# Optimization experiments

Measured on AMD Instinct MI355X. Metric: run time of the kernel, lower is better.

Reference implementation:

```python
import jax, jax.numpy as jnp
import numpy as np

B = 4096


def setup_inputs() -> dict:
    key = jax.random.key(0)
    u = jax.random.uniform(key, (B, 5), dtype=jnp.float32)
    centers = u[:, :2] * 64.0          # box centers in [0, 64)
    wh = u[:, 2:4] * 8.0 + 1.0         # widths/heights in [1, 9)
    ang = u[:, 4:5] * 3.14159265       # rotation angle in [0, pi)
    boxes = jnp.concatenate([centers, wh, ang], axis=-1)  # (B,5)
    return {"boxes": boxes}


def _rect_to_corners(boxes):
    # boxes: (B,5) = (x, y, w, h, theta) -> corners (B,4,2)
    unit = jnp.array([[-1.0, -1.0], [1.0, -1.0], [1.0, 1.0], [-1.0, 1.0]],
                     dtype=boxes.dtype)
    ctr, wh, ang = boxes[:, :2], boxes[:, 2:4], boxes[:, 4]
    base = unit[None, :, :] * (wh * 0.5)[:, None, :]        # (B,4,2)
    c, s = jnp.cos(ang), jnp.sin(ang)
    rot = jnp.stack([jnp.stack([c, -s], -1),
                     jnp.stack([s, c], -1)], axis=1)         # (B,2,2)
    return jnp.einsum('bkd,bde->bke', base, rot) + ctr[:, None, :]


def _giou1d(min1, max1, min2, max2):
    # exact (non-fast) 1-D GIoU per axis
    inter = jnp.clip(jnp.minimum(max1, max2) - jnp.maximum(min1, min2), 0.0)
    union = (max1 - min1) + (max2 - min2) - inter
    hull = jnp.maximum(max1, max2) - jnp.minimum(min1, min2)
    return inter / union - (hull - union) / hull


def reference(boxes):
    corners = _rect_to_corners(boxes)                        # (B,4,2)
    nb = corners.shape[0]
    # two edge axes per box: c1-c0 and c3-c0
    axes = jnp.stack([corners[:, 1] - corners[:, 0],
                      corners[:, 3] - corners[:, 0]], axis=1)  # (B,2,2)
    # self projections: box b's corners onto its own axes
    sp = jnp.einsum('bkd,bad->bak', corners, axes)           # (B,2,4)
    smin, smax = sp.min(-1), sp.max(-1)                      # (B,2)
    # cross projections: corners of box i onto axes of box j
    cp = jnp.einsum('ikd,jad->ijak', corners, axes)          # (B,B,2,4)
    cmin, cmax = cp.min(-1), cp.max(-1)                      # (B,B,2)
    # projections of box j's corners onto box i's axes = transpose of cross
    cminT, cmaxT = jnp.swapaxes(cmin, 0, 1), jnp.swapaxes(cmax, 0, 1)
    # axes of box i: (box i self) vs (box j projected on i's axes)
    gA = _giou1d(smin[:, None, :], smax[:, None, :], cminT, cmaxT)  # (B,B,2)
    # axes of box j: (box i projected on j's axes) vs (box j self)
    gB = _giou1d(cmin, cmax, smin[None, :, :], smax[None, :, :])    # (B,B,2)
    g = jnp.concatenate([gA, gB], axis=-1).min(-1)           # min over 4 axes
    pairwise = jnp.clip(g, 0.0)
    idx = jnp.arange(nb)
    pairwise = pairwise.at[idx, idx].set(0.0)                # zero diagonal
    return pairwise  # reduction='none' -> (B,B)
```

## Files before the change

kernel.cpp:

```cpp
#include <hip/hip_runtime.h>
#include <math.h>

#define NBOX 4096
#define TILE 32
#define NT (NBOX / TILE)
#define NBLK (NT * (NT + 1) / 2)
#define SS 12
#define JB 400

typedef float v2f __attribute__((ext_vector_type(2)));
typedef float vf4 __attribute__((ext_vector_type(4)));


struct Box {
    v2f A0, A1, SC, LL;
    float cx, cy;
};

__device__ __forceinline__ float rcp_fast(float x) { return __builtin_amdgcn_rcpf(x); }
__device__ __forceinline__ v2f splat(float s) { return (v2f){s, s}; }
__device__ __forceinline__ v2f fma2(v2f a, v2f b, v2f c) { return __builtin_elementwise_fma(a, b, c); }
__device__ __forceinline__ v2f abs2(v2f a) { return __builtin_elementwise_abs(a); }

__device__ __forceinline__ float mgiou_pair(const Box& I, const Box& J) {
    v2f dA = fma2(I.A0, splat(J.A0.x), I.A1 * J.A1.x);
    v2f dB = fma2(I.A0, splat(J.A0.y), I.A1 * J.A1.y);
    v2f DI = fma2(I.A0, splat(J.cx), fma2(I.A1, splat(J.cy), -I.SC));
    v2f DJ = fma2(J.A0, splat(I.cx), fma2(J.A1, splat(I.cy), -J.SC));
    v2f aA = abs2(dA), aB = abs2(dB);
    v2f HI = aA + aB;
    float HJ0 = aA.x + aA.y;
    float HJ1 = aB.x + aB.y;
    v2f SI = I.LL + HI;
    float SJ0 = J.LL.x + HJ0, SJ1 = J.LL.y + HJ1;
    v2f uI = fma2(splat(0.5f), SI, -abs2(DI));
    float uJ0 = fmaf(0.5f, SJ0, -fabsf(DJ.x));
    float uJ1 = fmaf(0.5f, SJ1, -fabsf(DJ.y));
    float r0 = fminf(fminf(I.LL.x, HI.x), uI.x);
    float r1 = fminf(fminf(I.LL.y, HI.y), uI.y);
    float r2 = fminf(fminf(J.LL.x, HJ0), uJ0);
    float r3 = fminf(fminf(J.LL.y, HJ1), uJ1);
    float g0 = r0 * rcp_fast(SI.x - r0);
    float g1 = r1 * rcp_fast(SI.y - r1);
    float g2 = r2 * rcp_fast(SJ0 - r2);
    float g3 = r3 * rcp_fast(SJ1 - r3);
    float g = fminf(fminf(g0, g1), fminf(g2, g3));
    return fmaxf(g, 0.0f);
}

__device__ __forceinline__ int sw_offset(int i) { return i * SS + (i >> 3) * 4; }

__device__ __forceinline__ Box load_box(const float* p) {
    Box b;
    float4 x = *(const float4*)(p);
    float4 y = *(const float4*)(p + 4);
    float2 z = *(const float2*)(p + 8);
    b.A0 = (v2f){x.x, x.y}; b.A1 = (v2f){x.z, x.w};
    b.SC = (v2f){y.x, y.y}; b.LL = (v2f){y.z, y.w};
    b.cx = z.x; b.cy = z.y;
    return b;
}

__global__ __launch_bounds__(64)
void pairwise_kernel(const float* __restrict__ boxes, float* __restrict__ out) {
    int k = blockIdx.x;
    int bi = (int)((float)(2 * NT + 1 - sqrtf((float)((2 * NT + 1) * (2 * NT + 1) - 8 * k))) * 0.5f);
    if (bi > 0 && k < bi * NT - bi * (bi - 1) / 2) bi--;
    if (k >= (bi + 1) * NT - (bi + 1) * bi / 2) bi++;
    int bj = bi + (k - (bi * NT - bi * (bi - 1) / 2));

    __shared__ float sm[JB + 400];

    int tid = threadIdx.x;
    {
        int loc = tid & (TILE - 1);
        int box = ((tid < TILE) ? bi : bj) * TILE + loc;
        float cx = boxes[box * 5 + 0];
        float cy = boxes[box * 5 + 1];
        float w  = boxes[box * 5 + 2];
        float h  = boxes[box * 5 + 3];
        float ang = boxes[box * 5 + 4];
        float s, c;
        __sincosf(ang, &s, &c);
        float a0x = w * c, a0y = -w * s;
        float a1x = h * s, a1y =  h * c;
        float sc0 = fmaf(a0x, cx, a0y * cy);
        float sc1 = fmaf(a1x, cx, a1y * cy);
        float* d = &sm[((tid < TILE) ? 0 : JB) + sw_offset(loc)];
        ((float4*)d)[0] = make_float4(a0x, a1x, a0y, a1y);
        ((float4*)d)[1] = make_float4(sc0, sc1, w * w, h * h);
        ((float2*)d)[4] = make_float2(cx, cy);
    }
    __syncthreads();

    int tx = tid & 7;
    int ty = tid >> 3;
    Box J[4];
    const float* jp = &sm[JB + sw_offset(4 * tx)];
    #pragma unroll
    for (int m = 0; m < 4; ++m) J[m] = load_box(jp + m * SS);

    int ibase = bi * TILE, jbase = bj * TILE;
    bool offdiag = (bi != bj);
    const float* ip = &sm[sw_offset(4 * ty)];
    float vT[4][4];

    #pragma unroll
    for (int kk = 0; kk < 4; ++kk) {
        Box I = load_box(ip + kk * SS);
        int ig = ibase + 4 * ty + kk;
        float v[4];
        #pragma unroll
        for (int m = 0; m < 4; ++m) {
            int jg = jbase + 4 * tx + m;
            v[m] = (ig == jg) ? 0.0f : mgiou_pair(I, J[m]);
            vT[m][kk] = v[m];
        }
        vf4 o = {v[0], v[1], v[2], v[3]};
        *(vf4*)&out[(size_t)ig * NBOX + jbase + 4 * tx] = o;
    }

    if (offdiag) {
        #pragma unroll
        for (int m = 0; m < 4; ++m) {
            int jg = jbase + 4 * tx + m;
            vf4 o = {vT[m][0], vT[m][1], vT[m][2], vT[m][3]};
            *(vf4*)&out[(size_t)jg * NBOX + ibase + 4 * ty] = o;
        }
    }
}

extern "C" void kernel_launch(void* const* d_in, const int* in_sizes, int n_in,
                              void* d_out, int out_size, void* d_ws, size_t ws_size,
                              hipStream_t stream) {
    const float* boxes = (const float*)d_in[0];
    float* out = (float*)d_out;
    pairwise_kernel<<<dim3(NBLK), dim3(64), 0, stream>>>(boxes, out);
}
```

Before: 80.98 us.

## Enlarge tiles to 128 and transpose mirrored block through shared memory

Raises the tile to 128 boxes with 1024-thread blocks and writes the mirrored (transposed) half through an XOR-swizzled shared-memory staging buffer. Each row store then becomes a contiguous row segment instead of short 16-byte strided pieces. The aim is better-coalesced global writes for the 64 MB output and less per-block setup. In exchange it needs a second barrier, about 76 KB of shared memory per block, and leaves far fewer blocks (528), which may underfill the GPU's compute units.

```diff
diff --git a/kernel.cpp b/kernel.cpp
--- a/kernel.cpp
+++ b/kernel.cpp
@@ -2,11 +2,13 @@
 #include <math.h>
 
 #define NBOX 4096
-#define TILE 32
+#define TILE 128
 #define NT (NBOX / TILE)
 #define NBLK (NT * (NT + 1) / 2)
 #define SS 12
-#define JB 400
+#define BOXREG 1600
+#define JB BOXREG
+#define TB (2 * BOXREG)
 
 typedef float v2f __attribute__((ext_vector_type(2)));
 typedef float vf4 __attribute__((ext_vector_type(4)));
@@ -61,7 +63,9 @@
     return b;
 }
 
-__global__ __launch_bounds__(64)
+__device__ __forceinline__ int tidx(int r, int c) { return TB + r * TILE + (c ^ (r & 28)); }
+
+__global__ __launch_bounds__(1024)
 void pairwise_kernel(const float* __restrict__ boxes, float* __restrict__ out) {
     int k = blockIdx.x;
     int bi = (int)((float)(2 * NT + 1 - sqrtf((float)((2 * NT + 1) * (2 * NT + 1) - 8 * k))) * 0.5f);
@@ -69,10 +73,10 @@
     if (k >= (bi + 1) * NT - (bi + 1) * bi / 2) bi++;
     int bj = bi + (k - (bi * NT - bi * (bi - 1) / 2));
 
-    __shared__ float sm[JB + 400];
+    __shared__ float sm[TB + TILE * TILE];
 
     int tid = threadIdx.x;
-    {
+    if (tid < 2 * TILE) {
         int loc = tid & (TILE - 1);
         int box = ((tid < TILE) ? bi : bj) * TILE + loc;
         float cx = boxes[box * 5 + 0];
@@ -93,39 +97,47 @@
     }
     __syncthreads();
 
-    int tx = tid & 7;
-    int ty = tid >> 3;
+    int wave = tid >> 6;
+    int lane = tid & 63;
+    int jq = lane & 31;
+    int iset = lane >> 5;
+    int rloc = 8 * wave + 4 * iset;
+
     Box J[4];
-    const float* jp = &sm[JB + sw_offset(4 * tx)];
+    const float* jp = &sm[JB + sw_offset(4 * jq)];
     #pragma unroll
     for (int m = 0; m < 4; ++m) J[m] = load_box(jp + m * SS);
 
     int ibase = bi * TILE, jbase = bj * TILE;
-    bool offdiag = (bi != bj);
-    const float* ip = &sm[sw_offset(4 * ty)];
+    const float* ip = &sm[sw_offset(rloc)];
     float vT[4][4];
 
     #pragma unroll
     for (int kk = 0; kk < 4; ++kk) {
         Box I = load_box(ip + kk * SS);
-        int ig = ibase + 4 * ty + kk;
-        float v[4];
+        int ig = ibase + rloc + kk;
         #pragma unroll
         for (int m = 0; m < 4; ++m) {
-            int jg = jbase + 4 * tx + m;
-            v[m] = (ig == jg) ? 0.0f : mgiou_pair(I, J[m]);
-            vT[m][kk] = v[m];
+            int jg = jbase + 4 * jq + m;
+            vT[m][kk] = (ig == jg) ? 0.0f : mgiou_pair(I, J[m]);
         }
-        vf4 o = {v[0], v[1], v[2], v[3]};
-        *(vf4*)&out[(size_t)ig * NBOX + jbase + 4 * tx] = o;
+        vf4 o = {vT[0][kk], vT[1][kk], vT[2][kk], vT[3][kk]};
+        *(vf4*)&out[(size_t)ig * NBOX + jbase + 4 * jq] = o;
     }
 
-    if (offdiag) {
+    if (bi != bj) {
         #pragma unroll
         for (int m = 0; m < 4; ++m) {
-            int jg = jbase + 4 * tx + m;
-            vf4 o = {vT[m][0], vT[m][1], vT[m][2], vT[m][3]};
-            *(vf4*)&out[(size_t)jg * NBOX + ibase + 4 * ty] = o;
+            int r = 4 * jq + m;
+            *(vf4*)&sm[tidx(r, rloc)] = (vf4){vT[m][0], vT[m][1], vT[m][2], vT[m][3]};
+        }
+        __syncthreads();
+        int cq = 4 * jq;
+        #pragma unroll
+        for (int q = 0; q < 4; ++q) {
+            int r2 = 8 * wave + 4 * iset + q;
+            vf4 o = *(const vf4*)&sm[tidx(r2, cq)];
+            *(vf4*)&out[(size_t)(jbase + r2) * NBOX + ibase + cq] = o;
         }
     }
 }
@@ -135,5 +147,5 @@
                               hipStream_t stream) {
     const float* boxes = (const float*)d_in[0];
     float* out = (float*)d_out;
-    pairwise_kernel<<<dim3(NBLK), dim3(64), 0, stream>>>(boxes, out);
+    pairwise_kernel<<<dim3(NBLK), dim3(1024), 0, stream>>>(boxes, out);
 }
```

Result: slower. 91.80 us (+13.4%).

## Pack J-box pairs for packed-FP32 math and replace four reciprocals with one

Applied to the files above, without the earlier changes.

Stores J boxes in shared memory as interleaved pairs so each thread evaluates two pairs at once with v2f packed FMA/min/max across the J dimension. The four per-axis ratio computations r/(S-r) are replaced by cross-multiplying onto a common denominator, so only one reciprocal per pair is needed. The diagonal check moves under a block-level diag flag. The common-denominator products can lose precision or overflow for extreme sizes, and they add extra multiplies.

```diff
diff --git a/kernel.cpp b/kernel.cpp
--- a/kernel.cpp
+++ b/kernel.cpp
@@ -7,58 +7,82 @@
 #define NBLK (NT * (NT + 1) / 2)
 #define SS 12
 #define JB 400
+#define JPS 20
 
 typedef float v2f __attribute__((ext_vector_type(2)));
 typedef float vf4 __attribute__((ext_vector_type(4)));
-
-
-struct Box {
-    v2f A0, A1, SC, LL;
-    float cx, cy;
-};
 
 __device__ __forceinline__ float rcp_fast(float x) { return __builtin_amdgcn_rcpf(x); }
 __device__ __forceinline__ v2f splat(float s) { return (v2f){s, s}; }
 __device__ __forceinline__ v2f fma2(v2f a, v2f b, v2f c) { return __builtin_elementwise_fma(a, b, c); }
 __device__ __forceinline__ v2f abs2(v2f a) { return __builtin_elementwise_abs(a); }
+__device__ __forceinline__ v2f min2(v2f a, v2f b) { return __builtin_elementwise_min(a, b); }
+__device__ __forceinline__ v2f max2(v2f a, v2f b) { return __builtin_elementwise_max(a, b); }
 
-__device__ __forceinline__ float mgiou_pair(const Box& I, const Box& J) {
-    v2f dA = fma2(I.A0, splat(J.A0.x), I.A1 * J.A1.x);
-    v2f dB = fma2(I.A0, splat(J.A0.y), I.A1 * J.A1.y);
-    v2f DI = fma2(I.A0, splat(J.cx), fma2(I.A1, splat(J.cy), -I.SC));
-    v2f DJ = fma2(J.A0, splat(I.cx), fma2(J.A1, splat(I.cy), -J.SC));
-    v2f aA = abs2(dA), aB = abs2(dB);
-    v2f HI = aA + aB;
-    float HJ0 = aA.x + aA.y;
-    float HJ1 = aB.x + aB.y;
-    v2f SI = I.LL + HI;
-    float SJ0 = J.LL.x + HJ0, SJ1 = J.LL.y + HJ1;
-    v2f uI = fma2(splat(0.5f), SI, -abs2(DI));
-    float uJ0 = fmaf(0.5f, SJ0, -fabsf(DJ.x));
-    float uJ1 = fmaf(0.5f, SJ1, -fabsf(DJ.y));
-    float r0 = fminf(fminf(I.LL.x, HI.x), uI.x);
-    float r1 = fminf(fminf(I.LL.y, HI.y), uI.y);
-    float r2 = fminf(fminf(J.LL.x, HJ0), uJ0);
-    float r3 = fminf(fminf(J.LL.y, HJ1), uJ1);
-    float g0 = r0 * rcp_fast(SI.x - r0);
-    float g1 = r1 * rcp_fast(SI.y - r1);
-    float g2 = r2 * rcp_fast(SJ0 - r2);
-    float g3 = r3 * rcp_fast(SJ1 - r3);
-    float g = fminf(fminf(g0, g1), fminf(g2, g3));
-    return fmaxf(g, 0.0f);
+struct IBox { float a0x, a1x, a0y, a1y, sc0, sc1, l0, l1, cx, cy; };
+struct PJ { v2f a0x, a1x, a0y, a1y, sc0, sc1, l0, l1, cx, cy; };
+
+__device__ __forceinline__ v2f mgiou_pair2(const IBox& I, const PJ& J) {
+    v2f d00 = fma2(splat(I.a0y), J.a0y, splat(I.a0x) * J.a0x);
+    v2f d01 = fma2(splat(I.a0y), J.a1y, splat(I.a0x) * J.a1x);
+    v2f d10 = fma2(splat(I.a1y), J.a0y, splat(I.a1x) * J.a0x);
+    v2f d11 = fma2(splat(I.a1y), J.a1y, splat(I.a1x) * J.a1x);
+    v2f DI0 = fma2(splat(I.a0x), J.cx, fma2(splat(I.a0y), J.cy, splat(-I.sc0)));
+    v2f DI1 = fma2(splat(I.a1x), J.cx, fma2(splat(I.a1y), J.cy, splat(-I.sc1)));
+    v2f DJ0 = fma2(J.a0x, splat(I.cx), fma2(J.a0y, splat(I.cy), -J.sc0));
+    v2f DJ1 = fma2(J.a1x, splat(I.cx), fma2(J.a1y, splat(I.cy), -J.sc1));
+    v2f a00 = abs2(d00), a01 = abs2(d01), a10 = abs2(d10), a11 = abs2(d11);
+    v2f HI0 = a00 + a01, HI1 = a10 + a11;
+    v2f HJ0 = a00 + a10, HJ1 = a01 + a11;
+    v2f SI0 = splat(I.l0) + HI0, SI1 = splat(I.l1) + HI1;
+    v2f SJ0 = J.l0 + HJ0, SJ1 = J.l1 + HJ1;
+    v2f uI0 = fma2(splat(0.5f), SI0, -abs2(DI0));
+    v2f uI1 = fma2(splat(0.5f), SI1, -abs2(DI1));
+    v2f uJ0 = fma2(splat(0.5f), SJ0, -abs2(DJ0));
+    v2f uJ1 = fma2(splat(0.5f), SJ1, -abs2(DJ1));
+    v2f rI0 = min2(min2(splat(I.l0), HI0), uI0);
+    v2f rI1 = min2(min2(splat(I.l1), HI1), uI1);
+    v2f rJ0 = min2(min2(J.l0, HJ0), uJ0);
+    v2f rJ1 = min2(min2(J.l1, HJ1), uJ1);
+    v2f S01 = SI0 * SI1, S23 = SJ0 * SJ1;
+    v2f P = S01 * S23;
+    v2f mI0 = rI0 * SI1 * S23;
+    v2f mI1 = rI1 * SI0 * S23;
+    v2f mJ0 = rJ0 * SJ1 * S01;
+    v2f mJ1 = rJ1 * SJ0 * S01;
+    v2f mm = min2(min2(mI0, mI1), min2(mJ0, mJ1));
+    mm = max2(mm, splat(0.0f));
+    v2f den = P - mm;
+    v2f r = {rcp_fast(den.x), rcp_fast(den.y)};
+    return mm * r;
 }
 
 __device__ __forceinline__ int sw_offset(int i) { return i * SS + (i >> 3) * 4; }
 
-__device__ __forceinline__ Box load_box(const float* p) {
-    Box b;
+__device__ __forceinline__ IBox load_ibox(const float* p) {
     float4 x = *(const float4*)(p);
     float4 y = *(const float4*)(p + 4);
     float2 z = *(const float2*)(p + 8);
-    b.A0 = (v2f){x.x, x.y}; b.A1 = (v2f){x.z, x.w};
-    b.SC = (v2f){y.x, y.y}; b.LL = (v2f){y.z, y.w};
+    IBox b;
+    b.a0x = x.x; b.a1x = x.y; b.a0y = x.z; b.a1y = x.w;
+    b.sc0 = y.x; b.sc1 = y.y; b.l0 = y.z; b.l1 = y.w;
     b.cx = z.x; b.cy = z.y;
     return b;
+}
+
+__device__ __forceinline__ PJ load_pj(const float* p) {
+    float4 q0 = *(const float4*)(p);
+    float4 q1 = *(const float4*)(p + 4);
+    float4 q2 = *(const float4*)(p + 8);
+    float4 q3 = *(const float4*)(p + 12);
+    float4 q4 = *(const float4*)(p + 16);
+    PJ j;
+    j.a0x = (v2f){q0.x, q0.y}; j.a1x = (v2f){q0.z, q0.w};
+    j.a0y = (v2f){q1.x, q1.y}; j.a1y = (v2f){q1.z, q1.w};
+    j.sc0 = (v2f){q2.x, q2.y}; j.sc1 = (v2f){q2.z, q2.w};
+    j.l0  = (v2f){q3.x, q3.y}; j.l1  = (v2f){q3.z, q3.w};
+    j.cx  = (v2f){q4.x, q4.y}; j.cy  = (v2f){q4.z, q4.w};
+    return j;
 }
 
 __global__ __launch_bounds__(64)
@@ -69,7 +93,7 @@
     if (k >= (bi + 1) * NT - (bi + 1) * bi / 2) bi++;
     int bj = bi + (k - (bi * NT - bi * (bi - 1) / 2));
 
-    __shared__ float sm[JB + 400];
+    __shared__ float sm[JB + 16 * JPS];
 
     int tid = threadIdx.x;
     {
@@ -86,41 +110,52 @@
         float a1x = h * s, a1y =  h * c;
         float sc0 = fmaf(a0x, cx, a0y * cy);
         float sc1 = fmaf(a1x, cx, a1y * cy);
-        float* d = &sm[((tid < TILE) ? 0 : JB) + sw_offset(loc)];
-        ((float4*)d)[0] = make_float4(a0x, a1x, a0y, a1y);
-        ((float4*)d)[1] = make_float4(sc0, sc1, w * w, h * h);
-        ((float2*)d)[4] = make_float2(cx, cy);
+        if (tid < TILE) {
+            float* d = &sm[sw_offset(loc)];
+            ((float4*)d)[0] = make_float4(a0x, a1x, a0y, a1y);
+            ((float4*)d)[1] = make_float4(sc0, sc1, w * w, h * h);
+            ((float2*)d)[4] = make_float2(cx, cy);
+        } else {
+            int p = loc >> 1, s2 = loc & 1;
+            float* d = &sm[JB + JPS * p + s2];
+            d[0]  = a0x; d[2]  = a1x; d[4]  = a0y; d[6]  = a1y;
+            d[8]  = sc0; d[10] = sc1; d[12] = w * w; d[14] = h * h;
+            d[16] = cx;  d[18] = cy;
+        }
     }
     __syncthreads();
 
     int tx = tid & 7;
     int ty = tid >> 3;
-    Box J[4];
-    const float* jp = &sm[JB + sw_offset(4 * tx)];
-    #pragma unroll
-    for (int m = 0; m < 4; ++m) J[m] = load_box(jp + m * SS);
+
+    PJ PJ0 = load_pj(&sm[JB + JPS * (2 * tx)]);
+    PJ PJ1 = load_pj(&sm[JB + JPS * (2 * tx + 1)]);
 
     int ibase = bi * TILE, jbase = bj * TILE;
-    bool offdiag = (bi != bj);
+    bool diag = (bi == bj);
     const float* ip = &sm[sw_offset(4 * ty)];
     float vT[4][4];
 
     #pragma unroll
     for (int kk = 0; kk < 4; ++kk) {
-        Box I = load_box(ip + kk * SS);
+        IBox I = load_ibox(ip + kk * SS);
         int ig = ibase + 4 * ty + kk;
-        float v[4];
-        #pragma unroll
-        for (int m = 0; m < 4; ++m) {
-            int jg = jbase + 4 * tx + m;
-            v[m] = (ig == jg) ? 0.0f : mgiou_pair(I, J[m]);
-            vT[m][kk] = v[m];
+        v2f g01 = mgiou_pair2(I, PJ0);
+        v2f g23 = mgiou_pair2(I, PJ1);
+        if (diag) {
+            int jg0 = jbase + 4 * tx;
+            if (ig == jg0)     g01.x = 0.0f;
+            if (ig == jg0 + 1) g01.y = 0.0f;
+            if (ig == jg0 + 2) g23.x = 0.0f;
+            if (ig == jg0 + 3) g23.y = 0.0f;
         }
-        vf4 o = {v[0], v[1], v[2], v[3]};
+        vT[0][kk] = g01.x; vT[1][kk] = g01.y;
+        vT[2][kk] = g23.x; vT[3][kk] = g23.y;
+        vf4 o = {g01.x, g01.y, g23.x, g23.y};
         *(vf4*)&out[(size_t)ig * NBOX + jbase + 4 * tx] = o;
     }
 
-    if (offdiag) {
+    if (!diag) {
         #pragma unroll
         for (int m = 0; m < 4; ++m) {
             int jg = jbase + 4 * tx + m;
```

Result: slower. 91.73 us (+13.3%).
